# Kernel tuning notes

Hardware: AMD Instinct MI355X
Metric: run time of the kernel (lower is better)

## Reference

```python
import jax, jax.numpy as jnp
import numpy as np

H, CH = 4, 16          # heads, hidden_features // heads
SLOPE = 0.2            # leaky_relu negative slope


def gat(x, W, a_src, a_dst):
    # x: (B, N, C); W: (hidden, C); a_src/a_dst: (H, CH)
    B, N, _ = x.shape
    h = (x @ W.T).reshape(B, N, H, CH)
    a1 = jnp.einsum('bnhc,hc->bnh', h, a_src)   # att_src scores
    a2 = jnp.einsum('bnhc,hc->bnh', h, a_dst)   # att_dst scores
    # torch: a1.unsqueeze(1) + a2.unsqueeze(2) -> (B, N, N, H)
    e = a1[:, None, :, :] + a2[:, :, None, :]
    e = jnp.transpose(e, (0, 3, 1, 2))          # (B, H, N, N)
    e = jnp.where(e >= 0, e, SLOPE * e)         # leaky_relu
    return jax.nn.softmax(e, axis=2)            # softmax over dim=2 as in torch


def pool(x, W1, b1, W2, b2):
    # diff-pool assignment: (B, N, K), then x' = S^T x -> (B, K, C)
    s = jax.nn.softmax(jax.nn.relu(x @ W1.T + b1) @ W2.T + b2, axis=-1)
    return jnp.einsum('bnk,bnc->bkc', s, x)


def fuse(att0, atts, lefts, rights):
    out = att0
    for a, l, r in zip(atts, lefts, rights):
        # left (H,J0,K) @ att (B,H,K,K) @ right (H,K,J0), broadcast over batch
        out = out + jnp.einsum('hjk,bhkl,hlm->bhjm', l, a, r)
    return out


def setup_inputs() -> dict:
    key = jax.random.key(0)
    ks = iter(jax.random.split(key, 40))
    n = lambda shape, s=0.1: jax.random.normal(next(ks), shape, dtype=jnp.float32) * s
    inp = {
        'src': n((64, 64, 64, 25), 1.0),
        'gat_lin': n((6, 64, 64)), 'gat_asrc': n((6, 4, 16)), 'gat_adst': n((6, 4, 16)),
        'sp0_W1': n((64, 64)), 'sp0_b1': jnp.zeros((64,), jnp.float32),
        'sp0_W2': n((12, 64)), 'sp0_b2': jnp.zeros((12,), jnp.float32),
        'sp1_W1': n((64, 64)), 'sp1_b1': jnp.zeros((64,), jnp.float32),
        'sp1_W2': n((5, 64)), 'sp1_b2': jnp.zeros((5,), jnp.float32),
        'tp0_W1': n((64, 64)), 'tp0_b1': jnp.zeros((64,), jnp.float32),
        'tp0_W2': n((32, 64)), 'tp0_b2': jnp.zeros((32,), jnp.float32),
        'tp1_W1': n((64, 64)), 'tp1_b1': jnp.zeros((64,), jnp.float32),
        'tp1_W2': n((12, 64)), 'tp1_b2': jnp.zeros((12,), jnp.float32),
        'sl0': n((4, 25, 12)), 'sr0': n((4, 12, 25)),
        'sl1': n((4, 25, 5)), 'sr1': n((4, 5, 25)),
        'tl0': n((4, 64, 32)), 'tr0': n((4, 32, 64)),
        'tl1': n((4, 64, 12)), 'tr1': n((4, 12, 64)),
    }
    return inp


def reference(src, gat_lin, gat_asrc, gat_adst,
              sp0_W1, sp0_b1, sp0_W2, sp0_b2, sp1_W1, sp1_b1, sp1_W2, sp1_b2,
              tp0_W1, tp0_b1, tp0_W2, tp0_b2, tp1_W1, tp1_b1, tp1_W2, tp1_b2,
              sl0, sr0, sl1, sr1, tl0, tr0, tl1, tr1):
    B, C, T, J = src.shape
    # ---- spatial branch: attention over joints per (batch, frame) ----
    xs = jnp.transpose(src, (0, 2, 3, 1)).reshape(B * T, J, C)
    a_s0 = gat(xs, gat_lin[0], gat_asrc[0], gat_adst[0])            # (BT,H,25,25)
    xs1 = pool(xs, sp0_W1, sp0_b1, sp0_W2, sp0_b2)                  # (BT,12,C)
    a_s1 = gat(xs1, gat_lin[1], gat_asrc[1], gat_adst[1])           # (BT,H,12,12)
    xs2 = pool(xs1, sp1_W1, sp1_b1, sp1_W2, sp1_b2)                 # (BT,5,C)
    a_s2 = gat(xs2, gat_lin[2], gat_asrc[2], gat_adst[2])           # (BT,H,5,5)
    s_fused = fuse(a_s0, [a_s1, a_s2], [sl0, sl1], [sr0, sr1])
    # ---- temporal branch: attention over frames per (batch, joint) ----
    xt = jnp.transpose(src, (0, 3, 2, 1)).reshape(B * J, T, C)
    a_t0 = gat(xt, gat_lin[3], gat_asrc[3], gat_adst[3])            # (BJ,H,64,64)
    xt1 = pool(xt, tp0_W1, tp0_b1, tp0_W2, tp0_b2)                  # (BJ,32,C)
    a_t1 = gat(xt1, gat_lin[4], gat_asrc[4], gat_adst[4])
    xt2 = pool(xt1, tp1_W1, tp1_b1, tp1_W2, tp1_b2)                 # (BJ,12,C)
    a_t2 = gat(xt2, gat_lin[5], gat_asrc[5], gat_adst[5])
    t_fused = fuse(a_t0, [a_t1, a_t2], [tl0, tl1], [tr0, tr1])
    return (s_fused.reshape(B, T, H, J, J), t_fused.reshape(B, J, H, T, T))
```

## Files before the change

### kernel.cpp

```cpp
#include <hip/hip_runtime.h>

#define DEVINL __device__ __forceinline__

DEVINL float leaky(float v) { return v >= 0.f ? v : 0.2f * v; }

__global__ void wprep_kernel(const float* __restrict__ lin,
                             const float* __restrict__ asrc,
                             const float* __restrict__ adst,
                             float* __restrict__ w_out) {
    int idx = blockIdx.x * blockDim.x + threadIdx.x;
    if (idx >= 6 * 4 * 64) return;
    int c = idx & 63;
    int h = (idx >> 6) & 3;
    int k = idx >> 8;
    const float* L = lin + k * 64 * 64;
    float s1 = 0.f, s2 = 0.f;
    for (int e = 0; e < 16; ++e) {
        float w = L[(h * 16 + e) * 64 + c];
        s1 += w * asrc[(k * 4 + h) * 16 + e];
        s2 += w * adst[(k * 4 + h) * 16 + e];
    }
    w_out[(k * 2 + 0) * 256 + h * 64 + c] = s1;
    w_out[(k * 2 + 1) * 256 + h * 64 + c] = s2;
}

__global__ void wtrans_kernel(const float* __restrict__ s0, const float* __restrict__ s1,
                              const float* __restrict__ t0, const float* __restrict__ t1,
                              const float* __restrict__ s0w2, const float* __restrict__ s1w2,
                              const float* __restrict__ t0w2, const float* __restrict__ t1w2,
                              float* __restrict__ o) {
    int idx = blockIdx.x * 256 + threadIdx.x;
    if (idx < 16384) {
        int m = idx >> 12, r = idx & 4095, c = r >> 6, d = r & 63;
        const float* src = (m == 0) ? s0 : (m == 1) ? s1 : (m == 2) ? t0 : t1;
        o[idx] = src[d * 64 + c];
    } else if (idx < 16384 + 768) {
        int j = idx - 16384, c = j / 12, k = j - 12 * c;
        o[idx] = s0w2[k * 64 + c];
    } else if (idx < 17152 + 512) {
        int j = idx - 17152, c = j >> 3, k = j & 7;
        o[idx] = (k < 5) ? s1w2[k * 64 + c] : 0.f;
    } else if (idx < 17664 + 2048) {
        int j = idx - 17664, c = j >> 5, k = j & 31;
        o[idx] = t0w2[k * 64 + c];
    } else if (idx < 19712 + 768) {
        int j = idx - 19712, c = j / 12, k = j - 12 * c;
        o[idx] = t1w2[k * 64 + c];
    }
}

template <int N, int K, int KP, int MODE, int WR>
__global__ __launch_bounds__(256) void pool_kernel(
    const float* __restrict__ x, const float* __restrict__ W1T,
    const float* __restrict__ b1, const float* __restrict__ W2T,
    const float* __restrict__ b2, const float* __restrict__ wsi,
    const float* __restrict__ wso, float* __restrict__ xo,
    float* __restrict__ sci, float* __restrict__ sco)
{
    constexpr int SLD = KP + 1;
    constexpr int XO_OFF = ((N * SLD + 3) & ~3);
    constexpr int SZT = (MODE == 1) ? 64 * 26 : (MODE == 2 ? 64 * 65 : 0);
    constexpr int R3A = XO_OFF + K * 68;
    constexpr int R3 = ((R3A > SZT ? R3A : SZT) + 3) & ~3;
    constexpr int TOT = 2 * N * 68 + R3 + 512;
    __shared__ float lds[TOT];
    float* xln = lds;
    float* yn  = lds + N * 68;
    float* r3  = yn + N * 68;
    float* sn  = r3;
    float* xoL = r3 + XO_OFF;
    float* wlo = r3 + R3;
    float* wli = yn;
    float* tile = r3;
    const int g = blockIdx.x, tid = threadIdx.x;

    if constexpr (MODE == 0) {
        const float4* xp = (const float4*)(x + (size_t)g * N * 64);
        for (int p = tid; p < N * 16; p += 256) {
            int n = p >> 4, c0 = (p & 15) << 2;
            *(float4*)&xln[n * 68 + c0] = xp[p];
        }
    } else if constexpr (MODE == 1) {
        int b = g >> 6, t = g & 63;
        const float* sp = x + b * 102400 + t * 25;
        for (int idx = tid; idx < 1600; idx += 256) {
            int c = idx / 25, j = idx - c * 25;
            tile[c * 26 + j] = sp[c * 1600 + j];
        }
        for (int i = tid; i < 512; i += 256) wli[i] = wsi[i];
    } else {
        int b = g / 25, j = g - b * 25;
        const float* sp = x + b * 102400 + j;
        for (int idx = tid; idx < 4096; idx += 256) {
            int c = idx >> 6, t = idx & 63;
            tile[c * 65 + t] = sp[c * 1600 + t * 25];
        }
        for (int i = tid; i < 512; i += 256) wli[i] = wsi[i];
    }
    for (int i = tid; i < 512; i += 256) wlo[i] = wso[i];
    __syncthreads();

    if constexpr (MODE != 0) {
        constexpr int TLD = (MODE == 1) ? 26 : 65;
        for (int p = tid; p < N * 64; p += 256) {
            int n = p >> 6, c = p & 63;
            xln[n * 68 + c] = tile[c * TLD + n];
        }
        __syncthreads();
        for (int p = tid; p < 8 * N; p += 256) {
            int q = p / N, n = p - q * N;
            const float* wv = wli + q * 64;
            const float* xr = &xln[n * 68];
            float acc = 0.f;
            #pragma unroll
            for (int c0 = 0; c0 < 64; c0 += 4) {
                float4 xv = *(const float4*)&xr[c0];
                float4 w4 = *(const float4*)&wv[c0];
                acc += xv.x * w4.x + xv.y * w4.y + xv.z * w4.z + xv.w * w4.w;
            }
            sci[(size_t)g * 8 * N + p] = acc;
        }
        __syncthreads();
    }

    for (int p = tid; p < N * 16; p += 256) {
        int n = p >> 4, d0 = (p & 15) << 2;
        const float* xr = &xln[n * 68];
        float4 bb = *(const float4*)(b1 + d0);
        float a0 = bb.x, a1 = bb.y, a2 = bb.z, a3 = bb.w;
        #pragma unroll 4
        for (int c0 = 0; c0 < 64; c0 += 4) {
            float4 xv = *(const float4*)&xr[c0];
            float4 w0 = *(const float4*)(W1T + (c0 + 0) * 64 + d0);
            float4 w1 = *(const float4*)(W1T + (c0 + 1) * 64 + d0);
            float4 w2 = *(const float4*)(W1T + (c0 + 2) * 64 + d0);
            float4 w3 = *(const float4*)(W1T + (c0 + 3) * 64 + d0);
            a0 += xv.x * w0.x + xv.y * w1.x + xv.z * w2.x + xv.w * w3.x;
            a1 += xv.x * w0.y + xv.y * w1.y + xv.z * w2.y + xv.w * w3.y;
            a2 += xv.x * w0.z + xv.y * w1.z + xv.z * w2.z + xv.w * w3.z;
            a3 += xv.x * w0.w + xv.y * w1.w + xv.z * w2.w + xv.w * w3.w;
        }
        *(float4*)&yn[n * 68 + d0] =
            make_float4(fmaxf(a0, 0.f), fmaxf(a1, 0.f), fmaxf(a2, 0.f), fmaxf(a3, 0.f));
    }
    __syncthreads();

    for (int p = tid; p < N * (KP / 4); p += 256) {
        int n = p / (KP / 4), k0 = (p % (KP / 4)) << 2;
        const float* yr = &yn[n * 68];
        float a0 = 0.f, a1 = 0.f, a2 = 0.f, a3 = 0.f;
        #pragma unroll 4
        for (int d0 = 0; d0 < 64; d0 += 4) {
            float4 yv = *(const float4*)&yr[d0];
            float4 w0 = *(const float4*)(W2T + (d0 + 0) * KP + k0);
            float4 w1 = *(const float4*)(W2T + (d0 + 1) * KP + k0);
            float4 w2 = *(const float4*)(W2T + (d0 + 2) * KP + k0);
            float4 w3 = *(const float4*)(W2T + (d0 + 3) * KP + k0);
            a0 += yv.x * w0.x + yv.y * w1.x + yv.z * w2.x + yv.w * w3.x;
            a1 += yv.x * w0.y + yv.y * w1.y + yv.z * w2.y + yv.w * w3.y;
            a2 += yv.x * w0.z + yv.y * w1.z + yv.z * w2.z + yv.w * w3.z;
            a3 += yv.x * w0.w + yv.y * w1.w + yv.z * w2.w + yv.w * w3.w;
        }
        float* sr = &sn[n * SLD + k0];
        sr[0] = (k0 + 0 < K) ? a0 + b2[k0 + 0] : -1e30f;
        sr[1] = (k0 + 1 < K) ? a1 + b2[k0 + 1] : -1e30f;
        sr[2] = (k0 + 2 < K) ? a2 + b2[k0 + 2] : -1e30f;
        sr[3] = (k0 + 3 < K) ? a3 + b2[k0 + 3] : -1e30f;
    }
    __syncthreads();

    if (tid < N) {
        float* sr = &sn[tid * SLD];
        float m = sr[0];
        #pragma unroll
        for (int k = 1; k < KP; ++k) m = fmaxf(m, sr[k]);
        float sum = 0.f;
        #pragma unroll
        for (int k = 0; k < KP; ++k) { float e = __expf(sr[k] - m); sr[k] = e; sum += e; }
        float inv = 1.f / sum;
        #pragma unroll
        for (int k = 0; k < KP; ++k) sr[k] *= inv;
    }
    __syncthreads();

    for (int p = tid; p < K * 16; p += 256) {
        int k = p >> 4, c0 = (p & 15) << 2;
        float a0 = 0.f, a1 = 0.f, a2 = 0.f, a3 = 0.f;
        for (int n = 0; n < N; ++n) {
            float s = sn[n * SLD + k];
            float4 xv = *(const float4*)&xln[n * 68 + c0];
            a0 += s * xv.x; a1 += s * xv.y; a2 += s * xv.z; a3 += s * xv.w;
        }
        float4 r = make_float4(a0, a1, a2, a3);
        *(float4*)&xoL[k * 68 + c0] = r;
        if constexpr (WR)
            *(float4*)(xo + (size_t)g * K * 64 + k * 64 + c0) = r;
    }
    __syncthreads();

    for (int p = tid; p < 8 * K; p += 256) {
        int q = p / K, k = p - q * K;
        const float* wv = wlo + q * 64;
        const float* xr = &xoL[k * 68];
        float acc = 0.f;
        #pragma unroll
        for (int c0 = 0; c0 < 64; c0 += 4) {
            float4 xv = *(const float4*)&xr[c0];
            float4 w4 = *(const float4*)&wv[c0];
            acc += xv.x * w4.x + xv.y * w4.y + xv.z * w4.z + xv.w * w4.w;
        }
        sco[(size_t)g * 8 * K + p] = acc;
    }
}

__global__ __launch_bounds__(256, 8) void gatfuse_t(
    const float* __restrict__ sc0,
    const float* __restrict__ sc1,
    const float* __restrict__ sc2,
    const float* __restrict__ L1,
    const float* __restrict__ R1,
    const float* __restrict__ L2,
    const float* __restrict__ R2,
    float* __restrict__ out)
{
    const int bid = blockIdx.x;
    const int g = (bid & 7) | ((bid >> 5) << 3);
    const int h = (bid >> 3) & 3;
    const int tid = threadIdx.x;
    __shared__ float t1T[32 * 64];
    __shared__ float t2T[12 * 64];
    __shared__ float A1[32 * 36];
    __shared__ float A2[12 * 13];
    __shared__ float4 row0[64], col0[64], row1[32], col1[32], row2[12], col2[12];
    __shared__ float mxs[3];

    if (tid < 64) col0[tid].x = sc0[((size_t)g * 8 + h) * 64 + tid];
    else if (tid < 128) row0[tid - 64].x = sc0[((size_t)g * 8 + 4 + h) * 64 + (tid - 64)];
    else if (tid < 160) col1[tid - 128].x = sc1[((size_t)g * 8 + h) * 32 + (tid - 128)];
    else if (tid < 192) row1[tid - 160].x = sc1[((size_t)g * 8 + 4 + h) * 32 + (tid - 160)];
    else if (tid < 204) col2[tid - 192].x = sc2[((size_t)g * 8 + h) * 12 + (tid - 192)];
    else if (tid < 216) row2[tid - 204].x = sc2[((size_t)g * 8 + 4 + h) * 12 + (tid - 204)];
    __syncthreads();

    if (tid < 64) {
        float mx = row0[0].x;
        for (int i = 1; i < 64; ++i) mx = fmaxf(mx, row0[i].x);
        if (tid == 0) mxs[0] = mx;
        float a = row0[tid].x;
        row0[tid] = make_float4(a, __expf(a - mx), __expf(0.2f * (a - mx)), 0.f);
    } else if (tid < 96) {
        float mx = row1[0].x;
        for (int k = 1; k < 32; ++k) mx = fmaxf(mx, row1[k].x);
        if (tid == 64) mxs[1] = mx;
        int k = tid - 64;
        float a = row1[k].x;
        row1[k] = make_float4(a, __expf(a - mx), __expf(0.2f * (a - mx)), 0.f);
    } else if (tid < 108) {
        float mx = row2[0].x;
        for (int k = 1; k < 12; ++k) mx = fmaxf(mx, row2[k].x);
        if (tid == 96) mxs[2] = mx;
        int k = tid - 96;
        float a = row2[k].x;
        row2[k] = make_float4(a, __expf(a - mx), __expf(0.2f * (a - mx)), 0.f);
    }
    __syncthreads();

    if (tid < 64) {
        float a = col0[tid].x, mx = mxs[0];
        float mj = leaky(a + mx);
        float Em = __expf(a + mx - mj);
        float Fm = __expf(0.2f * (a + mx) - mj);
        float S1 = 0.f, S2 = 0.f;
        for (int i = 0; i < 64; ++i) {
            float4 r = row0[i];
            bool c = (a + r.x >= 0.f);
            S1 += c ? r.y : 0.f;
            S2 += c ? 0.f : r.z;
        }
        float iv = 1.f / (Em * S1 + Fm * S2);
        col0[tid] = make_float4(a, Em * iv, Fm * iv, 0.f);
    } else if (tid < 96) {
        int l = tid - 64;
        float a = col1[l].x, mx = mxs[1];
        float mj = leaky(a + mx);
        float E = __expf(a + mx - mj);
        float F = __expf(0.2f * (a + mx) - mj);
        float S1 = 0.f, S2 = 0.f;
        for (int k = 0; k < 32; ++k) {
            float4 r = row1[k];
            bool c = (a + r.x >= 0.f);
            S1 += c ? r.y : 0.f;
            S2 += c ? 0.f : r.z;
        }
        float iv = 1.f / (E * S1 + F * S2);
        col1[l] = make_float4(a, E * iv, F * iv, 0.f);
    } else if (tid < 108) {
        int l = tid - 96;
        float a = col2[l].x, mx = mxs[2];
        float mj = leaky(a + mx);
        float E = __expf(a + mx - mj);
        float F = __expf(0.2f * (a + mx) - mj);
        float S1 = 0.f, S2 = 0.f;
        for (int k = 0; k < 12; ++k) {
            float4 r = row2[k];
            bool c = (a + r.x >= 0.f);
            S1 += c ? r.y : 0.f;
            S2 += c ? 0.f : r.z;
        }
        float iv = 1.f / (E * S1 + F * S2);
        col2[l] = make_float4(a, E * iv, F * iv, 0.f);
    }
    __syncthreads();

    #pragma unroll
    for (int q = 0; q < 4; ++q) {
        int idx = q * 256 + tid;
        int k = idx >> 5, l = idx & 31;
        float4 rk = row1[k];
        float4 cl = col1[l];
        A1[k * 36 + l] = (cl.x + rk.x >= 0.f) ? cl.y * rk.y : cl.z * rk.z;
    }
    if (tid < 144) {
        int k = tid / 12, l = tid - k * 12;
        float4 rk = row2[k];
        float4 cl = col2[l];
        A2[k * 13 + l] = (cl.x + rk.x >= 0.f) ? cl.y * rk.y : cl.z * rk.z;
    }
    __syncthreads();

    {
        const int j = tid & 63, l0 = (tid >> 6) * 8;
        const float* ljrow = L1 + ((size_t)h * 64 + j) * 32;
        float acc8[8] = {};
        for (int k = 0; k < 32; ++k) {
            float lk = ljrow[k];
            float4 a4a = *(const float4*)&A1[k * 36 + l0];
            float4 a4b = *(const float4*)&A1[k * 36 + l0 + 4];
            acc8[0] += lk * a4a.x; acc8[1] += lk * a4a.y;
            acc8[2] += lk * a4a.z; acc8[3] += lk * a4a.w;
            acc8[4] += lk * a4b.x; acc8[5] += lk * a4b.y;
            acc8[6] += lk * a4b.z; acc8[7] += lk * a4b.w;
        }
        #pragma unroll
        for (int lo = 0; lo < 8; ++lo) t1T[(l0 + lo) * 64 + j] = acc8[lo];
        const int lb = (tid >> 6) * 3;
        float lj2[12];
        const float4* lp2 = (const float4*)(L2 + ((size_t)h * 64 + j) * 12);
        #pragma unroll
        for (int q = 0; q < 3; ++q) {
            float4 v = lp2[q];
            lj2[q * 4] = v.x; lj2[q * 4 + 1] = v.y;
            lj2[q * 4 + 2] = v.z; lj2[q * 4 + 3] = v.w;
        }
        #pragma unroll
        for (int lo = 0; lo < 3; ++lo) {
            int l = lb + lo;
            float acc = 0.f;
            #pragma unroll
            for (int k = 0; k < 12; ++k) acc += lj2[k] * A2[k * 13 + l];
            t2T[l * 64 + j] = acc;
        }
    }
    __syncthreads();

    const int i0 = (tid >> 4) << 2, m0 = (tid & 15) << 2;
    float acc[4][4];
    {
        float4 cm[4] = {col0[m0], col0[m0 + 1], col0[m0 + 2], col0[m0 + 3]};
        float4 ri[4] = {row0[i0], row0[i0 + 1], row0[i0 + 2], row0[i0 + 3]};
        #pragma unroll
        for (int r = 0; r < 4; ++r)
            #pragma unroll
            for (int c = 0; c < 4; ++c)
                acc[r][c] = (cm[c].x + ri[r].x >= 0.f) ? cm[c].y * ri[r].y
                                                       : cm[c].z * ri[r].z;
    }
    const float* r1b = R1 + (size_t)h * 2048;
    #pragma unroll 8
    for (int l = 0; l < 32; ++l) {
        float4 t4 = *(const float4*)&t1T[l * 64 + i0];
        float4 r4 = *(const float4*)(r1b + l * 64 + m0);
        float tv[4] = {t4.x, t4.y, t4.z, t4.w};
        float rv[4] = {r4.x, r4.y, r4.z, r4.w};
        #pragma unroll
        for (int r = 0; r < 4; ++r)
            #pragma unroll
            for (int c = 0; c < 4; ++c) acc[r][c] += tv[r] * rv[c];
    }
    const float* r2b = R2 + (size_t)h * 768;
    #pragma unroll 4
    for (int l = 0; l < 12; ++l) {
        float4 t4 = *(const float4*)&t2T[l * 64 + i0];
        float4 r4 = *(const float4*)(r2b + l * 64 + m0);
        float tv[4] = {t4.x, t4.y, t4.z, t4.w};
        float rv[4] = {r4.x, r4.y, r4.z, r4.w};
        #pragma unroll
        for (int r = 0; r < 4; ++r)
            #pragma unroll
            for (int c = 0; c < 4; ++c) acc[r][c] += tv[r] * rv[c];
    }
    float* op = out + ((size_t)g * 4 + h) * 4096;
    #pragma unroll
    for (int r = 0; r < 4; ++r)
        *(float4*)&op[(i0 + r) * 64 + m0] =
            make_float4(acc[r][0], acc[r][1], acc[r][2], acc[r][3]);
}

__global__ __launch_bounds__(256, 5) void gatfuse_s(
    const float* __restrict__ sc0,
    const float* __restrict__ sc1,
    const float* __restrict__ sc2,
    const float* __restrict__ L1,
    const float* __restrict__ R1,
    const float* __restrict__ L2,
    const float* __restrict__ R2,
    float* __restrict__ out)
{
    const int g = blockIdx.x;
    const int tid = threadIdx.x;
    const int h = tid >> 6, t = tid & 63;
    __shared__ float4 row0[4][25], col0[4][25];
    __shared__ float4 row1[4][12], col1[4][12];
    __shared__ float4 row2[4][5], col2[4][5];
    __shared__ float A1[4][12 * 13];
    __shared__ float A2[4][5 * 6];
    __shared__ float t1l[4][25 * 16];
    __shared__ float t2l[4][25 * 8];
    __shared__ float r1T[4][25 * 16];
    __shared__ float r2T[4][25 * 8];
    __shared__ float mxs[4][3];

    for (int p = t; p < 84; p += 64) {
        if (p < 25)      col0[h][p].x      = sc0[((size_t)g * 8 + h) * 25 + p];
        else if (p < 50) row0[h][p - 25].x = sc0[((size_t)g * 8 + 4 + h) * 25 + (p - 25)];
        else if (p < 62) col1[h][p - 50].x = sc1[((size_t)g * 8 + h) * 12 + (p - 50)];
        else if (p < 74) row1[h][p - 62].x = sc1[((size_t)g * 8 + 4 + h) * 12 + (p - 62)];
        else if (p < 79) col2[h][p - 74].x = sc2[((size_t)g * 8 + h) * 5 + (p - 74)];
        else             row2[h][p - 79].x = sc2[((size_t)g * 8 + 4 + h) * 5 + (p - 79)];
    }
    for (int idx = t; idx < 400; idx += 64) {
        int m = idx >> 4, l = idx & 15;
        r1T[h][idx] = (l < 12) ? R1[h * 300 + l * 25 + m] : 0.f;
    }
    for (int idx = t; idx < 200; idx += 64) {
        int m = idx >> 3, l = idx & 7;
        r2T[h][idx] = (l < 5) ? R2[h * 125 + l * 25 + m] : 0.f;
    }
    __syncthreads();

    if (t < 25) {
        float mx = row0[h][0].x;
        for (int i = 1; i < 25; ++i) mx = fmaxf(mx, row0[h][i].x);
        if (t == 0) mxs[h][0] = mx;
        float a = row0[h][t].x;
        row0[h][t] = make_float4(a, __expf(a - mx), __expf(0.2f * (a - mx)), 0.f);
    } else if (t >= 32 && t < 44) {
        float mx = row1[h][0].x;
        for (int k = 1; k < 12; ++k) mx = fmaxf(mx, row1[h][k].x);
        if (t == 32) mxs[h][1] = mx;
        int k = t - 32;
        float a = row1[h][k].x;
        row1[h][k] = make_float4(a, __expf(a - mx), __expf(0.2f * (a - mx)), 0.f);
    } else if (t >= 48 && t < 53) {
        float mx = row2[h][0].x;
        for (int k = 1; k < 5; ++k) mx = fmaxf(mx, row2[h][k].x);
        if (t == 48) mxs[h][2] = mx;
        int k = t - 48;
        float a = row2[h][k].x;
        row2[h][k] = make_float4(a, __expf(a - mx), __expf(0.2f * (a - mx)), 0.f);
    }
    __syncthreads();

    if (t < 25) {
        float a = col0[h][t].x, mx = mxs[h][0];
        float mj = leaky(a + mx);
        float E = __expf(a + mx - mj);
        float F = __expf(0.2f * (a + mx) - mj);
        float S1 = 0.f, S2 = 0.f;
        for (int i = 0; i < 25; ++i) {
            float4 r = row0[h][i];
            bool c = (a + r.x >= 0.f);
            S1 += c ? r.y : 0.f;
            S2 += c ? 0.f : r.z;
        }
        float iv = 1.f / (E * S1 + F * S2);
        col0[h][t] = make_float4(a, E * iv, F * iv, 0.f);
    } else if (t >= 32 && t < 44) {
        int l = t - 32;
        float a = col1[h][l].x, mx = mxs[h][1];
        float mj = leaky(a + mx);
        float E = __expf(a + mx - mj);
        float F = __expf(0.2f * (a + mx) - mj);
        float S1 = 0.f, S2 = 0.f;
        for (int k = 0; k < 12; ++k) {
            float4 r = row1[h][k];
            bool c = (a + r.x >= 0.f);
            S1 += c ? r.y : 0.f;
            S2 += c ? 0.f : r.z;
        }
        float iv = 1.f / (E * S1 + F * S2);
        col1[h][l] = make_float4(a, E * iv, F * iv, 0.f);
    } else if (t >= 48 && t < 53) {
        int l = t - 48;
        float a = col2[h][l].x, mx = mxs[h][2];
        float mj = leaky(a + mx);
        float E = __expf(a + mx - mj);
        float F = __expf(0.2f * (a + mx) - mj);
        float S1 = 0.f, S2 = 0.f;
        for (int k = 0; k < 5; ++k) {
            float4 r = row2[h][k];
            bool c = (a + r.x >= 0.f);
            S1 += c ? r.y : 0.f;
            S2 += c ? 0.f : r.z;
        }
        float iv = 1.f / (E * S1 + F * S2);
        col2[h][l] = make_float4(a, E * iv, F * iv, 0.f);
    }
    __syncthreads();

    for (int p = t; p < 144; p += 64) {
        int k = p / 12, l = p - k * 12;
        float4 rk = row1[h][k];
        float4 cl = col1[h][l];
        A1[h][k * 13 + l] = (cl.x + rk.x >= 0.f) ? cl.y * rk.y : cl.z * rk.z;
    }
    if (t < 25) {
        int k = t / 5, l = t - (t / 5) * 5;
        float4 rk = row2[h][k];
        float4 cl = col2[h][l];
        A2[h][k * 6 + l] = (cl.x + rk.x >= 0.f) ? cl.y * rk.y : cl.z * rk.z;
    }
    __syncthreads();

    if (t < 25) {
        float lj[12];
        const float4* lp = (const float4*)(L1 + ((size_t)h * 25 + t) * 12);
        #pragma unroll
        for (int q = 0; q < 3; ++q) {
            float4 v = lp[q];
            lj[q * 4] = v.x; lj[q * 4 + 1] = v.y; lj[q * 4 + 2] = v.z; lj[q * 4 + 3] = v.w;
        }
        #pragma unroll
        for (int l = 0; l < 12; ++l) {
            float acc = 0.f;
            #pragma unroll
            for (int k = 0; k < 12; ++k) acc += lj[k] * A1[h][k * 13 + l];
            t1l[h][t * 16 + l] = acc;
        }
        #pragma unroll
        for (int l = 12; l < 16; ++l) t1l[h][t * 16 + l] = 0.f;
        float lj2[5];
        const float* lp2 = L2 + ((size_t)h * 25 + t) * 5;
        #pragma unroll
        for (int k = 0; k < 5; ++k) lj2[k] = lp2[k];
        #pragma unroll
        for (int l = 0; l < 5; ++l) {
            float acc = 0.f;
            #pragma unroll
            for (int k = 0; k < 5; ++k) acc += lj2[k] * A2[h][k * 6 + l];
            t2l[h][t * 8 + l] = acc;
        }
        #pragma unroll
        for (int l = 5; l < 8; ++l) t2l[h][t * 8 + l] = 0.f;
    }
    __syncthreads();

    float* op = out + ((size_t)g * 4 + h) * 625;
    for (int idx = t; idx < 625; idx += 64) {
        int i = idx / 25, m = idx - i * 25;
        float4 cm = col0[h][m];
        float4 ri = row0[h][i];
        float val = (cm.x + ri.x >= 0.f) ? cm.y * ri.y : cm.z * ri.z;
        const float* t1r = &t1l[h][i * 16];
        const float* r1c = &r1T[h][m * 16];
        #pragma unroll
        for (int q = 0; q < 4; ++q) {
            float4 tv = *(const float4*)&t1r[q * 4];
            float4 rv = *(const float4*)&r1c[q * 4];
            val += tv.x * rv.x + tv.y * rv.y + tv.z * rv.z + tv.w * rv.w;
        }
        const float* t2r = &t2l[h][i * 8];
        const float* r2c = &r2T[h][m * 8];
        #pragma unroll
        for (int q = 0; q < 2; ++q) {
            float4 tv = *(const float4*)&t2r[q * 4];
            float4 rv = *(const float4*)&r2c[q * 4];
            val += tv.x * rv.x + tv.y * rv.y + tv.z * rv.z + tv.w * rv.w;
        }
        op[idx] = val;
    }
}

extern "C" void kernel_launch(void* const* d_in, const int* in_sizes, int n_in,
                              void* d_out, int out_size, void* d_ws, size_t ws_size,
                              hipStream_t stream) {
    const float* src    = (const float*)d_in[0];
    const float* lin    = (const float*)d_in[1];
    const float* asrc   = (const float*)d_in[2];
    const float* adst   = (const float*)d_in[3];
    const float* sp0_W1 = (const float*)d_in[4];
    const float* sp0_b1 = (const float*)d_in[5];
    const float* sp0_W2 = (const float*)d_in[6];
    const float* sp0_b2 = (const float*)d_in[7];
    const float* sp1_W1 = (const float*)d_in[8];
    const float* sp1_b1 = (const float*)d_in[9];
    const float* sp1_W2 = (const float*)d_in[10];
    const float* sp1_b2 = (const float*)d_in[11];
    const float* tp0_W1 = (const float*)d_in[12];
    const float* tp0_b1 = (const float*)d_in[13];
    const float* tp0_W2 = (const float*)d_in[14];
    const float* tp0_b2 = (const float*)d_in[15];
    const float* tp1_W1 = (const float*)d_in[16];
    const float* tp1_b1 = (const float*)d_in[17];
    const float* tp1_W2 = (const float*)d_in[18];
    const float* tp1_b2 = (const float*)d_in[19];
    const float* sl0    = (const float*)d_in[20];
    const float* sr0    = (const float*)d_in[21];
    const float* sl1    = (const float*)d_in[22];
    const float* sr1    = (const float*)d_in[23];
    const float* tl0    = (const float*)d_in[24];
    const float* tr0    = (const float*)d_in[25];
    const float* tl1    = (const float*)d_in[26];
    const float* tr1    = (const float*)d_in[27];

    float* out_s = (float*)d_out;
    float* out_t = out_s + 10240000;

    float* ws   = (float*)d_ws;
    float* wbuf = ws;
    float* wT   = ws + 4096;

    float* sp0_W1T = wT;
    float* sp1_W1T = wT + 4096;
    float* tp0_W1T = wT + 8192;
    float* tp1_W1T = wT + 12288;
    float* sp0_W2T = wT + 16384;
    float* sp1_W2T = wT + 17152;
    float* tp0_W2T = wT + 17664;
    float* tp1_W2T = wT + 19712;

    float* a = ws + 24576;
    float* xs1  = a;              a += 3145728;
    float* xt1  = a;              a += 3276800;
    float* scS0 = a;              a += 819200;
    float* scS1 = a;              a += 393216;
    float* scS2 = a;              a += 163840;
    float* scT0 = a;              a += 819200;
    float* scT1 = a;              a += 409600;
    float* scT2 = a;              a += 153600;

    wprep_kernel<<<6, 256, 0, stream>>>(lin, asrc, adst, wbuf);
    wtrans_kernel<<<80, 256, 0, stream>>>(sp0_W1, sp1_W1, tp0_W1, tp1_W1,
                                          sp0_W2, sp1_W2, tp0_W2, tp1_W2, wT);

    pool_kernel<25, 12, 12, 1, 1><<<4096, 256, 0, stream>>>(
        src, sp0_W1T, sp0_b1, sp0_W2T, sp0_b2,
        wbuf + 0 * 512, wbuf + 1 * 512, xs1, scS0, scS1);
    pool_kernel<12, 5, 8, 0, 0><<<4096, 256, 0, stream>>>(
        xs1, sp1_W1T, sp1_b1, sp1_W2T, sp1_b2,
        nullptr, wbuf + 2 * 512, nullptr, nullptr, scS2);
    gatfuse_s<<<4096, 256, 0, stream>>>(scS0, scS1, scS2, sl0, sr0, sl1, sr1, out_s);

    pool_kernel<64, 32, 32, 2, 1><<<1600, 256, 0, stream>>>(
        src, tp0_W1T, tp0_b1, tp0_W2T, tp0_b2,
        wbuf + 3 * 512, wbuf + 4 * 512, xt1, scT0, scT1);
    pool_kernel<32, 12, 12, 0, 0><<<1600, 256, 0, stream>>>(
        xt1, tp1_W1T, tp1_b1, tp1_W2T, tp1_b2,
        nullptr, wbuf + 5 * 512, nullptr, nullptr, scT2);
    gatfuse_t<<<6400, 256, 0, stream>>>(scT0, scT1, scT2, tl0, tr0, tl1, tr1, out_t);
}
```

Before: 435.1 us.

## Split transpose into separate kernels and chunk pool hidden layer to cut LDS

Moves the src transpose and first-level attention-score computation out of pool_kernel into dedicated xs/xt kernels that write a transposed copy of the input to global memory. The pool kernel now always reads contiguous rows and computes the hidden layer in chunks of NH rows, shrinking its shared-memory footprint, and it carries a launch-bounds occupancy hint. Workspace buffers are reused between the spatial and temporal branches. The intent is higher occupancy in the pool kernels, paid for with an extra global round-trip of the transposed input and two more launches.

```diff
diff --git a/kernel.cpp b/kernel.cpp
--- a/kernel.cpp
+++ b/kernel.cpp
@@ -49,125 +49,139 @@
     }
 }
 
-template <int N, int K, int KP, int MODE, int WR>
-__global__ __launch_bounds__(256) void pool_kernel(
+__global__ __launch_bounds__(256) void xs_kernel(
+    const float* __restrict__ src, const float* __restrict__ w,
+    float* __restrict__ xs, float* __restrict__ sc) {
+    int g = blockIdx.x;
+    int b = g >> 6, t = g & 63;
+    __shared__ float tile[64 * 26];
+    __shared__ float wl[512];
+    const float* sp = src + b * 102400 + t * 25;
+    for (int idx = threadIdx.x; idx < 1600; idx += 256) {
+        int c = idx / 25, j = idx - c * 25;
+        tile[c * 26 + j] = sp[c * 1600 + j];
+    }
+    for (int i = threadIdx.x; i < 512; i += 256) wl[i] = w[i];
+    __syncthreads();
+    float* op = xs + (size_t)g * 1600;
+    for (int idx = threadIdx.x; idx < 1600; idx += 256) {
+        int j = idx >> 6, c = idx & 63;
+        op[idx] = tile[c * 26 + j];
+    }
+    for (int p = threadIdx.x; p < 200; p += 256) {
+        int q = p / 25, n = p - q * 25;
+        const float* wp = wl + q * 64;
+        float acc = 0.f;
+        #pragma unroll 8
+        for (int c = 0; c < 64; ++c) acc += tile[c * 26 + n] * wp[c];
+        sc[(size_t)g * 200 + p] = acc;
+    }
+}
+
+__global__ __launch_bounds__(256) void xt_kernel(
+    const float* __restrict__ src, const float* __restrict__ w,
+    float* __restrict__ xt, float* __restrict__ sc) {
+    int g = blockIdx.x;
+    int b = g / 25, j = g - b * 25;
+    __shared__ float tile[64 * 65];
+    __shared__ float wl[512];
+    const float* sp = src + b * 102400 + j;
+    for (int idx = threadIdx.x; idx < 4096; idx += 256) {
+        int c = idx >> 6, t = idx & 63;
+        tile[c * 65 + t] = sp[c * 1600 + t * 25];
+    }
+    for (int i = threadIdx.x; i < 512; i += 256) wl[i] = w[i];
+    __syncthreads();
+    float* op = xt + (size_t)g * 4096;
+    for (int idx = threadIdx.x; idx < 4096; idx += 256) {
+        int t = idx >> 6, c = idx & 63;
+        op[idx] = tile[c * 65 + t];
+    }
+    for (int p = threadIdx.x; p < 512; p += 256) {
+        int q = p >> 6, n = p & 63;
+        const float* wp = wl + q * 64;
+        float acc = 0.f;
+        #pragma unroll 8
+        for (int c = 0; c < 64; ++c) acc += tile[c * 65 + n] * wp[c];
+        sc[(size_t)g * 512 + p] = acc;
+    }
+}
+
+template <int N, int NH, int K, int KP, int WR>
+__global__ __launch_bounds__(256, 3) void pool_kernel(
     const float* __restrict__ x, const float* __restrict__ W1T,
     const float* __restrict__ b1, const float* __restrict__ W2T,
-    const float* __restrict__ b2, const float* __restrict__ wsi,
-    const float* __restrict__ wso, float* __restrict__ xo,
-    float* __restrict__ sci, float* __restrict__ sco)
+    const float* __restrict__ b2, const float* __restrict__ wso,
+    float* __restrict__ xo, float* __restrict__ sco)
 {
+    static_assert(K <= NH && (N % NH) == 0, "layout");
     constexpr int SLD = KP + 1;
-    constexpr int XO_OFF = ((N * SLD + 3) & ~3);
-    constexpr int SZT = (MODE == 1) ? 64 * 26 : (MODE == 2 ? 64 * 65 : 0);
-    constexpr int R3A = XO_OFF + K * 68;
-    constexpr int R3 = ((R3A > SZT ? R3A : SZT) + 3) & ~3;
-    constexpr int TOT = 2 * N * 68 + R3 + 512;
-    __shared__ float lds[TOT];
+    constexpr int YH = N * 68;
+    constexpr int SN = YH + NH * 68;
+    constexpr int WLO = SN + N * SLD;
+    __shared__ float lds[WLO + 512];
     float* xln = lds;
-    float* yn  = lds + N * 68;
-    float* r3  = yn + N * 68;
-    float* sn  = r3;
-    float* xoL = r3 + XO_OFF;
-    float* wlo = r3 + R3;
-    float* wli = yn;
-    float* tile = r3;
+    float* yh  = lds + YH;
+    float* sn  = lds + SN;
+    float* wlo = lds + WLO;
+    float* xoL = yh;
     const int g = blockIdx.x, tid = threadIdx.x;
 
-    if constexpr (MODE == 0) {
-        const float4* xp = (const float4*)(x + (size_t)g * N * 64);
-        for (int p = tid; p < N * 16; p += 256) {
-            int n = p >> 4, c0 = (p & 15) << 2;
-            *(float4*)&xln[n * 68 + c0] = xp[p];
-        }
-    } else if constexpr (MODE == 1) {
-        int b = g >> 6, t = g & 63;
-        const float* sp = x + b * 102400 + t * 25;
-        for (int idx = tid; idx < 1600; idx += 256) {
-            int c = idx / 25, j = idx - c * 25;
-            tile[c * 26 + j] = sp[c * 1600 + j];
-        }
-        for (int i = tid; i < 512; i += 256) wli[i] = wsi[i];
-    } else {
-        int b = g / 25, j = g - b * 25;
-        const float* sp = x + b * 102400 + j;
-        for (int idx = tid; idx < 4096; idx += 256) {
-            int c = idx >> 6, t = idx & 63;
-            tile[c * 65 + t] = sp[c * 1600 + t * 25];
-        }
-        for (int i = tid; i < 512; i += 256) wli[i] = wsi[i];
+    const float4* xp = (const float4*)(x + (size_t)g * N * 64);
+    for (int p = tid; p < N * 16; p += 256) {
+        int n = p >> 4, c0 = (p & 15) << 2;
+        *(float4*)&xln[n * 68 + c0] = xp[p];
     }
     for (int i = tid; i < 512; i += 256) wlo[i] = wso[i];
     __syncthreads();
 
-    if constexpr (MODE != 0) {
-        constexpr int TLD = (MODE == 1) ? 26 : 65;
-        for (int p = tid; p < N * 64; p += 256) {
-            int n = p >> 6, c = p & 63;
-            xln[n * 68 + c] = tile[c * TLD + n];
-        }
-        __syncthreads();
-        for (int p = tid; p < 8 * N; p += 256) {
-            int q = p / N, n = p - q * N;
-            const float* wv = wli + q * 64;
-            const float* xr = &xln[n * 68];
-            float acc = 0.f;
-            #pragma unroll
+    #pragma unroll
+    for (int h0 = 0; h0 < N; h0 += NH) {
+        for (int p = tid; p < NH * 16; p += 256) {
+            int nl = p >> 4, d0 = (p & 15) << 2;
+            const float* xr = &xln[(h0 + nl) * 68];
+            float4 bb = *(const float4*)(b1 + d0);
+            float a0 = bb.x, a1 = bb.y, a2 = bb.z, a3 = bb.w;
+            #pragma unroll 4
             for (int c0 = 0; c0 < 64; c0 += 4) {
                 float4 xv = *(const float4*)&xr[c0];
-                float4 w4 = *(const float4*)&wv[c0];
-                acc += xv.x * w4.x + xv.y * w4.y + xv.z * w4.z + xv.w * w4.w;
+                float4 w0 = *(const float4*)(W1T + (c0 + 0) * 64 + d0);
+                float4 w1 = *(const float4*)(W1T + (c0 + 1) * 64 + d0);
+                float4 w2 = *(const float4*)(W1T + (c0 + 2) * 64 + d0);
+                float4 w3 = *(const float4*)(W1T + (c0 + 3) * 64 + d0);
+                a0 += xv.x * w0.x + xv.y * w1.x + xv.z * w2.x + xv.w * w3.x;
+                a1 += xv.x * w0.y + xv.y * w1.y + xv.z * w2.y + xv.w * w3.y;
+                a2 += xv.x * w0.z + xv.y * w1.z + xv.z * w2.z + xv.w * w3.z;
+                a3 += xv.x * w0.w + xv.y * w1.w + xv.z * w2.w + xv.w * w3.w;
             }
-            sci[(size_t)g * 8 * N + p] = acc;
+            *(float4*)&yh[nl * 68 + d0] =
+                make_float4(fmaxf(a0, 0.f), fmaxf(a1, 0.f), fmaxf(a2, 0.f), fmaxf(a3, 0.f));
         }
         __syncthreads();
-    }
-
-    for (int p = tid; p < N * 16; p += 256) {
-        int n = p >> 4, d0 = (p & 15) << 2;
-        const float* xr = &xln[n * 68];
-        float4 bb = *(const float4*)(b1 + d0);
-        float a0 = bb.x, a1 = bb.y, a2 = bb.z, a3 = bb.w;
-        #pragma unroll 4
-        for (int c0 = 0; c0 < 64; c0 += 4) {
-            float4 xv = *(const float4*)&xr[c0];
-            float4 w0 = *(const float4*)(W1T + (c0 + 0) * 64 + d0);
-            float4 w1 = *(const float4*)(W1T + (c0 + 1) * 64 + d0);
-            float4 w2 = *(const float4*)(W1T + (c0 + 2) * 64 + d0);
-            float4 w3 = *(const float4*)(W1T + (c0 + 3) * 64 + d0);
-            a0 += xv.x * w0.x + xv.y * w1.x + xv.z * w2.x + xv.w * w3.x;
-            a1 += xv.x * w0.y + xv.y * w1.y + xv.z * w2.y + xv.w * w3.y;
-            a2 += xv.x * w0.z + xv.y * w1.z + xv.z * w2.z + xv.w * w3.z;
-            a3 += xv.x * w0.w + xv.y * w1.w + xv.z * w2.w + xv.w * w3.w;
-        }
-        *(float4*)&yn[n * 68 + d0] =
-            make_float4(fmaxf(a0, 0.f), fmaxf(a1, 0.f), fmaxf(a2, 0.f), fmaxf(a3, 0.f));
-    }
-    __syncthreads();
-
-    for (int p = tid; p < N * (KP / 4); p += 256) {
-        int n = p / (KP / 4), k0 = (p % (KP / 4)) << 2;
-        const float* yr = &yn[n * 68];
-        float a0 = 0.f, a1 = 0.f, a2 = 0.f, a3 = 0.f;
-        #pragma unroll 4
-        for (int d0 = 0; d0 < 64; d0 += 4) {
-            float4 yv = *(const float4*)&yr[d0];
-            float4 w0 = *(const float4*)(W2T + (d0 + 0) * KP + k0);
-            float4 w1 = *(const float4*)(W2T + (d0 + 1) * KP + k0);
-            float4 w2 = *(const float4*)(W2T + (d0 + 2) * KP + k0);
-            float4 w3 = *(const float4*)(W2T + (d0 + 3) * KP + k0);
-            a0 += yv.x * w0.x + yv.y * w1.x + yv.z * w2.x + yv.w * w3.x;
-            a1 += yv.x * w0.y + yv.y * w1.y + yv.z * w2.y + yv.w * w3.y;
-            a2 += yv.x * w0.z + yv.y * w1.z + yv.z * w2.z + yv.w * w3.z;
-            a3 += yv.x * w0.w + yv.y * w1.w + yv.z * w2.w + yv.w * w3.w;
-        }
-        float* sr = &sn[n * SLD + k0];
-        sr[0] = (k0 + 0 < K) ? a0 + b2[k0 + 0] : -1e30f;
-        sr[1] = (k0 + 1 < K) ? a1 + b2[k0 + 1] : -1e30f;
-        sr[2] = (k0 + 2 < K) ? a2 + b2[k0 + 2] : -1e30f;
-        sr[3] = (k0 + 3 < K) ? a3 + b2[k0 + 3] : -1e30f;
-    }
-    __syncthreads();
+        for (int p = tid; p < NH * (KP / 4); p += 256) {
+            int nl = p / (KP / 4), k0 = (p % (KP / 4)) << 2;
+            const float* yr = &yh[nl * 68];
+            float a0 = 0.f, a1 = 0.f, a2 = 0.f, a3 = 0.f;
+            #pragma unroll 4
+            for (int d0 = 0; d0 < 64; d0 += 4) {
+                float4 yv = *(const float4*)&yr[d0];
+                float4 w0 = *(const float4*)(W2T + (d0 + 0) * KP + k0);
+                float4 w1 = *(const float4*)(W2T + (d0 + 1) * KP + k0);
+                float4 w2 = *(const float4*)(W2T + (d0 + 2) * KP + k0);
+                float4 w3 = *(const float4*)(W2T + (d0 + 3) * KP + k0);
+                a0 += yv.x * w0.x + yv.y * w1.x + yv.z * w2.x + yv.w * w3.x;
+                a1 += yv.x * w0.y + yv.y * w1.y + yv.z * w2.y + yv.w * w3.y;
+                a2 += yv.x * w0.z + yv.y * w1.z + yv.z * w2.z + yv.w * w3.z;
+                a3 += yv.x * w0.w + yv.y * w1.w + yv.z * w2.w + yv.w * w3.w;
+            }
+            float* sr = &sn[(h0 + nl) * SLD + k0];
+            sr[0] = (k0 + 0 < K) ? a0 + b2[k0 + 0] : -1e30f;
+            sr[1] = (k0 + 1 < K) ? a1 + b2[k0 + 1] : -1e30f;
+            sr[2] = (k0 + 2 < K) ? a2 + b2[k0 + 2] : -1e30f;
+            sr[3] = (k0 + 3 < K) ? a3 + b2[k0 + 3] : -1e30f;
+        }
+        __syncthreads();
+    }
 
     if (tid < N) {
         float* sr = &sn[tid * SLD];
@@ -639,33 +653,27 @@
     float* tp0_W2T = wT + 17664;
     float* tp1_W2T = wT + 19712;
 
-    float* a = ws + 24576;
-    float* xs1  = a;              a += 3145728;
-    float* xt1  = a;              a += 3276800;
-    float* scS0 = a;              a += 819200;
-    float* scS1 = a;              a += 393216;
-    float* scS2 = a;              a += 163840;
-    float* scT0 = a;              a += 819200;
-    float* scT1 = a;              a += 409600;
-    float* scT2 = a;              a += 153600;
+    float* xbuf  = ws + 24576;
+    float* x1buf = xbuf + 6553600;
+    float* sc0b  = x1buf + 3276800;
+    float* sc1b  = sc0b + 819200;
+    float* sc2b  = sc1b + 409600;
 
     wprep_kernel<<<6, 256, 0, stream>>>(lin, asrc, adst, wbuf);
     wtrans_kernel<<<80, 256, 0, stream>>>(sp0_W1, sp1_W1, tp0_W1, tp1_W1,
                                           sp0_W2, sp1_W2, tp0_W2, tp1_W2, wT);
 
-    pool_kernel<25, 12, 12, 1, 1><<<4096, 256, 0, stream>>>(
-        src, sp0_W1T, sp0_b1, sp0_W2T, sp0_b2,
-        wbuf + 0 * 512, wbuf + 1 * 512, xs1, scS0, scS1);
-    pool_kernel<12, 5, 8, 0, 0><<<4096, 256, 0, stream>>>(
-        xs1, sp1_W1T, sp1_b1, sp1_W2T, sp1_b2,
-        nullptr, wbuf + 2 * 512, nullptr, nullptr, scS2);
-    gatfuse_s<<<4096, 256, 0, stream>>>(scS0, scS1, scS2, sl0, sr0, sl1, sr1, out_s);
-
-    pool_kernel<64, 32, 32, 2, 1><<<1600, 256, 0, stream>>>(
-        src, tp0_W1T, tp0_b1, tp0_W2T, tp0_b2,
-        wbuf + 3 * 512, wbuf + 4 * 512, xt1, scT0, scT1);
-    pool_kernel<32, 12, 12, 0, 0><<<1600, 256, 0, stream>>>(
-        xt1, tp1_W1T, tp1_b1, tp1_W2T, tp1_b2,
-        nullptr, wbuf + 5 * 512, nullptr, nullptr, scT2);
-    gatfuse_t<<<6400, 256, 0, stream>>>(scT0, scT1, scT2, tl0, tr0, tl1, tr1, out_t);
-}
+    xs_kernel<<<4096, 256, 0, stream>>>(src, wbuf + 0 * 512, xbuf, sc0b);
+    pool_kernel<25, 25, 12, 12, 1><<<4096, 256, 0, stream>>>(
+        xbuf, sp0_W1T, sp0_b1, sp0_W2T, sp0_b2, wbuf + 1 * 512, x1buf, sc1b);
+    pool_kernel<12, 12, 5, 8, 0><<<4096, 256, 0, stream>>>(
+        x1buf, sp1_W1T, sp1_b1, sp1_W2T, sp1_b2, wbuf + 2 * 512, nullptr, sc2b);
+    gatfuse_s<<<4096, 256, 0, stream>>>(sc0b, sc1b, sc2b, sl0, sr0, sl1, sr1, out_s);
+
+    xt_kernel<<<1600, 256, 0, stream>>>(src, wbuf + 3 * 512, xbuf, sc0b);
+    pool_kernel<64, 32, 32, 32, 1><<<1600, 256, 0, stream>>>(
+        xbuf, tp0_W1T, tp0_b1, tp0_W2T, tp0_b2, wbuf + 4 * 512, x1buf, sc1b);
+    pool_kernel<32, 32, 12, 12, 0><<<1600, 256, 0, stream>>>(
+        x1buf, tp1_W1T, tp1_b1, tp1_W2T, tp1_b2, wbuf + 5 * 512, nullptr, sc2b);
+    gatfuse_t<<<6400, 256, 0, stream>>>(sc0b, sc1b, sc2b, tl0, tr0, tl1, tr1, out_t);
+}
```

New measurement: 463.4 us. 1.06x slower.
